# Optimization experiments

Hardware: AMD Instinct MI355X
Metric: run time of the kernel (lower is better)

Reference implementation:

```python
import jax, jax.numpy as jnp
import numpy as np

N_NODES = 100000
N_EDGES = 3200000
IN_CH, HIDDEN, OUT_CH = 256, 16, 16


def setup_inputs() -> dict:
    key = jax.random.key(0)
    k1, k2, k3, k4, k5, k6 = jax.random.split(key, 6)
    x = jax.random.normal(k1, (N_NODES, IN_CH), dtype=jnp.float32)
    edge_index = jax.random.randint(k2, (2, N_EDGES), 0, N_NODES, dtype=jnp.int64)
    W1 = jax.random.normal(k3, (IN_CH, HIDDEN), dtype=jnp.float32) * (1.0 / np.sqrt(IN_CH))
    b1 = jax.random.normal(k4, (HIDDEN,), dtype=jnp.float32) * 0.01
    W2 = jax.random.normal(k5, (HIDDEN, OUT_CH), dtype=jnp.float32) * (1.0 / np.sqrt(HIDDEN))
    b2 = jax.random.normal(k6, (OUT_CH,), dtype=jnp.float32) * 0.01
    return {"x": x, "edge_index": edge_index, "W1": W1, "b1": b1, "W2": W2, "b2": b2}


def gcn_layer(x, edge_index, W, b):
    # Linear projection: [N, in] @ [in, out] + b
    h = x @ W + b
    source, target = edge_index[0], edge_index[1]
    n = x.shape[0]
    # degree of target nodes (in-degree), symmetric normalization (Kipf & Welling 2017)
    deg = jax.ops.segment_sum(jnp.ones_like(target, dtype=h.dtype), target, num_segments=n)
    deg_inv_sqrt = jnp.where(deg > 0, jax.lax.rsqrt(jnp.maximum(deg, 1.0)), 0.0)
    norm = deg_inv_sqrt[source] * deg_inv_sqrt[target]  # [E]
    # gather-scale-scatter: msg = norm * h[source], aggregated by add at target
    msgs = norm[:, None] * h[source]  # [E, out]
    return jax.ops.segment_sum(msgs, target, num_segments=n)


def reference(x, edge_index, W1, b1, W2, b2):
    h = jax.nn.sigmoid(gcn_layer(x, edge_index, W1, b1))
    return jax.nn.sigmoid(gcn_layer(h, edge_index, W2, b2))
```

## Files before the change

kernel.cpp:

```cpp
#include <hip/hip_runtime.h>
#include <hip/hip_bf16.h>

#define IN_CH 256
#define HID 16
#define BS 256
#define CAP 9216
#define CHUNK 4096
#define PBLK 512
#define EPT (CHUNK/PBLK)
#define SORT_CAP CAP

typedef __attribute__((ext_vector_type(8))) short bf16x8;
typedef __attribute__((ext_vector_type(4))) float floatx4;

static __device__ __forceinline__ short f2bf(float f) {
    __hip_bfloat16 h = __float2bfloat16(f);
    return *reinterpret_cast<short*>(&h);
}

static __device__ __forceinline__ void acc8(float* a, uint4 v) {
    unsigned w;
    w = v.x;
    a[0] += __uint_as_float(w << 16);
    a[1] += __uint_as_float(w & 0xffff0000u);
    w = v.y;
    a[2] += __uint_as_float(w << 16);
    a[3] += __uint_as_float(w & 0xffff0000u);
    w = v.z;
    a[4] += __uint_as_float(w << 16);
    a[5] += __uint_as_float(w & 0xffff0000u);
    w = v.w;
    a[6] += __uint_as_float(w << 16);
    a[7] += __uint_as_float(w & 0xffff0000u);
}

__global__ __launch_bounds__(PBLK) void k_part(
        const int* __restrict__ src, const int* __restrict__ tgt,
        int* __restrict__ gcursor, unsigned int* __restrict__ csr, int E, int nbuk) {
    __shared__ int lcount[512];
    __shared__ int lexcl[512];
    __shared__ int gspan[512];
    __shared__ unsigned int sepk[CHUNK];
    __shared__ unsigned short sbuk[CHUNK];
    __shared__ int stot;
    int t = threadIdx.x;
    int base = blockIdx.x * CHUNK;

    lcount[t] = 0;
    __syncthreads();

    int ebuk[EPT], eofs[EPT];
    unsigned epk[EPT];
#pragma unroll
    for (int k = 0; k < EPT; k++) {
        int e = base + t + k * PBLK;
        if (e < E) {
            int s  = __builtin_nontemporal_load(src + e);
            int tg = __builtin_nontemporal_load(tgt + e);
            ebuk[k] = tg >> 8;
            epk[k] = ((unsigned)s << 8) | (unsigned)(tg & 255);
            eofs[k] = atomicAdd(&lcount[ebuk[k]], 1);
        } else {
            ebuk[k] = -1;
        }
    }
    __syncthreads();
    int v = lcount[t];
    lexcl[t] = v;
    __syncthreads();
    for (int off = 1; off < 512; off <<= 1) {
        int a = (t >= off) ? lexcl[t - off] : 0;
        __syncthreads();
        lexcl[t] += a;
        __syncthreads();
    }
    int inc = lexcl[t];
    if (t == 511) stot = inc;
    if (t < nbuk && v > 0) gspan[t] = atomicAdd(&gcursor[t], v);
    __syncthreads();
    lexcl[t] = inc - v;
    __syncthreads();
#pragma unroll
    for (int k = 0; k < EPT; k++) {
        if (ebuk[k] >= 0) {
            int sp = lexcl[ebuk[k]] + eofs[k];
            sepk[sp] = epk[k];
            sbuk[sp] = (unsigned short)ebuk[k];
        }
    }
    __syncthreads();
    int total = stot;
    for (int p = t; p < total; p += PBLK) {
        int buk = sbuk[p];
        int gp = gspan[buk] + (p - lexcl[buk]);
        if (gp < CAP)
            csr[(size_t)buk * CAP + gp] = sepk[p];
    }
}

__global__ __launch_bounds__(512, 4) void k_sortgemm(
        const unsigned int* __restrict__ csr, const int* __restrict__ gcursor,
        const float* __restrict__ x, const float* __restrict__ W1,
        const float* __restrict__ b1,
        int* __restrict__ csr2, int* __restrict__ rowptr,
        int* __restrict__ deg, float* __restrict__ dis,
        short* __restrict__ h1, int N) {
    __shared__ int lcnt[256];
    __shared__ int lscan[256];
    __shared__ float sdis[256];
    __shared__ int ssrc[SORT_CAP];
    int t = threadIdx.x, b = blockIdx.x;
    int start = b * CAP;
    int cnt = min(gcursor[b], CAP);
    int end = start + cnt;

    if (t < 256) lcnt[t] = 0;
    __syncthreads();
    for (int p = start + t; p < end; p += 512) atomicAdd(&lcnt[csr[p] & 255], 1);
    __syncthreads();
    int d = 0;
    if (t < 256) { d = lcnt[t]; lscan[t] = d; }
    __syncthreads();
    for (int off = 1; off < 256; off <<= 1) {
        int a = 0;
        if (t < 256 && t >= off) a = lscan[t - off];
        __syncthreads();
        if (t < 256) lscan[t] += a;
        __syncthreads();
    }
    if (t < 256) {
        int excl = lscan[t] - d;
        int n = b * BS + t;
        float dv = (d > 0) ? rsqrtf((float)d) : 0.0f;
        sdis[t] = dv;
        if (n < N) {
            rowptr[n] = start + excl;
            deg[n] = d;
            dis[n] = dv;
        }
        lcnt[t] = excl;
    }
    __syncthreads();
    for (int p = start + t; p < end; p += 512) {
        unsigned pk = csr[p];
        int pos = atomicAdd(&lcnt[pk & 255], 1);
        ssrc[pos] = (int)(pk >> 8);
    }
    __syncthreads();
    for (int i = t; i < cnt; i += 512) csr2[start + i] = ssrc[i];

    {
        int lane = t & 63, wave = t >> 6;
        int mc = lane & 15, q = lane >> 4;
        bf16x8 bfrag[8];
#pragma unroll
        for (int kb = 0; kb < 8; kb++) {
#pragma unroll
            for (int j = 0; j < 8; j++)
                bfrag[kb][j] = f2bf(W1[(kb * 32 + q * 8 + j) * HID + mc]);
        }
        float bias = b1[mc];
#pragma unroll
        for (int r2 = 0; r2 < 2; r2++) {
            int nb = b * BS + (wave * 2 + r2) * 16;
            if (nb < N) {
                const float* xrow = x + (size_t)(nb + mc) * IN_CH;
                floatx4 acc = {0.f, 0.f, 0.f, 0.f};
#pragma unroll
                for (int kb = 0; kb < 8; kb++) {
                    const floatx4* p = (const floatx4*)(xrow + kb * 32 + q * 8);
                    floatx4 v0 = __builtin_nontemporal_load(p);
                    floatx4 v1 = __builtin_nontemporal_load(p + 1);
                    bf16x8 afrag;
#pragma unroll
                    for (int j = 0; j < 4; j++) {
                        afrag[j]     = f2bf(v0[j]);
                        afrag[j + 4] = f2bf(v1[j]);
                    }
                    acc = __builtin_amdgcn_mfma_f32_16x16x32_bf16(afrag, bfrag[kb], acc, 0, 0, 0);
                }
#pragma unroll
                for (int r = 0; r < 4; r++) {
                    int node = nb + q * 4 + r;
                    h1[(size_t)node * HID + mc] = f2bf((acc[r] + bias) * sdis[node - b * BS]);
                }
            }
        }
    }
}

__global__ __launch_bounds__(256) void k_agg_mid(
        const short* __restrict__ h1, const int* __restrict__ csr2,
        const int* __restrict__ rowptr, const int* __restrict__ deg,
        const float* __restrict__ dis,
        const float* __restrict__ W2, const float* __restrict__ b2,
        short* __restrict__ h2, int N) {
    __shared__ float w2s[256];
    __shared__ float b2s[16];
    __shared__ float sv[32][17];
    int t = threadIdx.x;
    w2s[t] = W2[t];
    if (t < 16) b2s[t] = b2[t];
    int nl  = t >> 3;
    int sub = t & 7;
    int cg  = sub & 1;
    int par = sub >> 1;
    int n = blockIdx.x * 32 + nl;

    float a[8] = {0.f, 0.f, 0.f, 0.f, 0.f, 0.f, 0.f, 0.f};
    float d = 0.f;
    if (n < N) {
        d = dis[n];
        int start = rowptr[n], cnt = deg[n];
        const short* hb = h1 + 8 * cg;
        int i = start + par, end = start + cnt;
        for (; i + 4 < end; i += 8) {
            int s0 = csr2[i], s1 = csr2[i + 4];
            uint4 v0 = *(const uint4*)(hb + 16 * (size_t)s0);
            uint4 v1 = *(const uint4*)(hb + 16 * (size_t)s1);
            acc8(a, v0); acc8(a, v1);
        }
        if (i < end) {
            uint4 v = *(const uint4*)(hb + 16 * (size_t)csr2[i]);
            acc8(a, v);
        }
    }
#pragma unroll
    for (int j = 0; j < 8; j++) {
        a[j] += __shfl_xor(a[j], 2);
        a[j] += __shfl_xor(a[j], 4);
    }
    sv[nl][8 * cg + 2 * par]     = 1.0f / (1.0f + __expf(-d * a[2 * par]));
    sv[nl][8 * cg + 2 * par + 1] = 1.0f / (1.0f + __expf(-d * a[2 * par + 1]));
    __syncthreads();
    if (n < N) {
        int oc = sub * 2;
        float o0 = b2s[oc], o1 = b2s[oc + 1];
#pragma unroll
        for (int k = 0; k < 16; k++) {
            float s = sv[nl][k];
            o0 += s * w2s[k * 16 + oc];
            o1 += s * w2s[k * 16 + oc + 1];
        }
        unsigned pk = ((unsigned)(unsigned short)f2bf(o1 * d) << 16)
                    | (unsigned)(unsigned short)f2bf(o0 * d);
        *(unsigned int*)(h2 + 16 * (size_t)n + oc) = pk;
    }
}

__global__ __launch_bounds__(256) void k_agg_out(
        const short* __restrict__ h2, const int* __restrict__ csr2,
        const int* __restrict__ rowptr, const int* __restrict__ deg,
        const float* __restrict__ dis, float* __restrict__ out, int N) {
    int t = threadIdx.x;
    int nl  = t >> 3;
    int sub = t & 7;
    int cg  = sub & 1;
    int par = sub >> 1;
    int n = blockIdx.x * 32 + nl;
    if (n >= N) return;
    float d = dis[n];
    int start = rowptr[n], cnt = deg[n];
    float a[8] = {0.f, 0.f, 0.f, 0.f, 0.f, 0.f, 0.f, 0.f};
    const short* hb = h2 + 8 * cg;
    int i = start + par, end = start + cnt;
    for (; i + 4 < end; i += 8) {
        int s0 = csr2[i], s1 = csr2[i + 4];
        uint4 v0 = *(const uint4*)(hb + 16 * (size_t)s0);
        uint4 v1 = *(const uint4*)(hb + 16 * (size_t)s1);
        acc8(a, v0); acc8(a, v1);
    }
    if (i < end) {
        uint4 v = *(const uint4*)(hb + 16 * (size_t)csr2[i]);
        acc8(a, v);
    }
#pragma unroll
    for (int j = 0; j < 8; j++) {
        a[j] += __shfl_xor(a[j], 2);
        a[j] += __shfl_xor(a[j], 4);
    }
    float2 o;
    o.x = 1.0f / (1.0f + __expf(-d * a[2 * par]));
    o.y = 1.0f / (1.0f + __expf(-d * a[2 * par + 1]));
    *(float2*)(out + 16 * (size_t)n + 8 * cg + 2 * par) = o;
}

extern "C" void kernel_launch(void* const* d_in, const int* in_sizes, int n_in,
                              void* d_out, int out_size, void* d_ws, size_t ws_size,
                              hipStream_t stream) {
    const float* x  = (const float*)d_in[0];
    const int*   ei = (const int*)d_in[1];
    const float* W1 = (const float*)d_in[2];
    const float* b1 = (const float*)d_in[3];
    const float* W2 = (const float*)d_in[4];
    const float* b2 = (const float*)d_in[5];
    float* out = (float*)d_out;

    int N = in_sizes[0] / IN_CH;
    int E = in_sizes[1] / 2;
    const int* src = ei;
    const int* tgt = ei + E;

    int NBUK = (N + BS - 1) / BS;

    char* ws = (char*)d_ws;
    auto align256 = [](size_t v) { return (v + 255) & ~(size_t)255; };
    size_t off = 0;
    int*          gcursor = (int*)(ws + off);          off += align256(512 * sizeof(int));
    unsigned int* csr     = (unsigned int*)(ws + off); off += align256((size_t)NBUK * CAP * sizeof(unsigned int));
    int*          csr2    = (int*)(ws + off);          off += align256((size_t)NBUK * CAP * sizeof(int));
    int*          rowptr  = (int*)(ws + off);          off += align256((size_t)N * sizeof(int));
    int*          deg     = (int*)(ws + off);          off += align256((size_t)N * sizeof(int));
    float*        dis     = (float*)(ws + off);        off += align256((size_t)N * sizeof(float));
    short*        h1      = (short*)(ws + off);        off += align256((size_t)N * HID * sizeof(short));
    short*        h2      = (short*)(ws + off);        off += align256((size_t)N * HID * sizeof(short));

    int grid_part = (E + CHUNK - 1) / CHUNK;
    int grid_ag   = (N + 31) / 32;

    hipMemsetAsync(gcursor, 0, 512 * sizeof(int), stream);
    k_part    <<<grid_part, PBLK, 0, stream>>>(src, tgt, gcursor, csr, E, NBUK);
    k_sortgemm<<<NBUK, 512, 0, stream>>>(csr, gcursor, x, W1, b1,
                                         csr2, rowptr, deg, dis, h1, N);
    k_agg_mid <<<grid_ag, 256, 0, stream>>>(h1, csr2, rowptr, deg, dis, W2, b2, h2, N);
    k_agg_out <<<grid_ag, 256, 0, stream>>>(h2, csr2, rowptr, deg, dis, out, N);
}
```

Baseline: 265.6 us.

## Store layer-1 features as FP8 and enlarge partition chunk size

The layer-1 projected features h1 are now stored as FP8 (one byte per channel) instead of bf16. That halves the gather traffic in the first aggregation, and each thread decodes a full 16-channel row with packed fp8-to-f32 conversions. The reduction across the 8 lanes per node becomes a butterfly transpose-reduce so each lane ends up owning two channels. The partition chunk size per block is also doubled. FP8 storage of the normalized features adds substantial quantization error, which may break accuracy tolerances.

Result: faster. 255.7 us (-3.7%).

```diff
diff --git a/kernel.cpp b/kernel.cpp
--- a/kernel.cpp
+++ b/kernel.cpp
@@ -5,13 +5,14 @@
 #define HID 16
 #define BS 256
 #define CAP 9216
-#define CHUNK 4096
+#define CHUNK 8192
 #define PBLK 512
 #define EPT (CHUNK/PBLK)
 #define SORT_CAP CAP
 
 typedef __attribute__((ext_vector_type(8))) short bf16x8;
 typedef __attribute__((ext_vector_type(4))) float floatx4;
+typedef __attribute__((ext_vector_type(2))) float floatx2;
 
 static __device__ __forceinline__ short f2bf(float f) {
     __hip_bfloat16 h = __float2bfloat16(f);
@@ -34,6 +35,18 @@
     a[7] += __uint_as_float(w & 0xffff0000u);
 }
 
+static __device__ __forceinline__ void dec16(float* a, uint4 v) {
+    floatx2 f;
+    f = __builtin_amdgcn_cvt_pk_f32_fp8((int)v.x, false); a[0] += f[0];  a[1] += f[1];
+    f = __builtin_amdgcn_cvt_pk_f32_fp8((int)v.x, true ); a[2] += f[0];  a[3] += f[1];
+    f = __builtin_amdgcn_cvt_pk_f32_fp8((int)v.y, false); a[4] += f[0];  a[5] += f[1];
+    f = __builtin_amdgcn_cvt_pk_f32_fp8((int)v.y, true ); a[6] += f[0];  a[7] += f[1];
+    f = __builtin_amdgcn_cvt_pk_f32_fp8((int)v.z, false); a[8] += f[0];  a[9] += f[1];
+    f = __builtin_amdgcn_cvt_pk_f32_fp8((int)v.z, true ); a[10] += f[0]; a[11] += f[1];
+    f = __builtin_amdgcn_cvt_pk_f32_fp8((int)v.w, false); a[12] += f[0]; a[13] += f[1];
+    f = __builtin_amdgcn_cvt_pk_f32_fp8((int)v.w, true ); a[14] += f[0]; a[15] += f[1];
+}
+
 __global__ __launch_bounds__(PBLK) void k_part(
         const int* __restrict__ src, const int* __restrict__ tgt,
         int* __restrict__ gcursor, unsigned int* __restrict__ csr, int E, int nbuk) {
@@ -104,7 +117,7 @@
         const float* __restrict__ b1,
         int* __restrict__ csr2, int* __restrict__ rowptr,
         int* __restrict__ deg, float* __restrict__ dis,
-        short* __restrict__ h1, int N) {
+        unsigned char* __restrict__ h1, int N) {
     __shared__ int lcnt[256];
     __shared__ int lscan[256];
     __shared__ float sdis[256];
@@ -182,7 +195,9 @@
 #pragma unroll
                 for (int r = 0; r < 4; r++) {
                     int node = nb + q * 4 + r;
-                    h1[(size_t)node * HID + mc] = f2bf((acc[r] + bias) * sdis[node - b * BS]);
+                    float val = (acc[r] + bias) * sdis[node - b * BS];
+                    int pkv = __builtin_amdgcn_cvt_pk_fp8_f32(val, val, 0, false);
+                    h1[(size_t)node * HID + mc] = (unsigned char)(pkv & 0xff);
                 }
             }
         }
@@ -190,7 +205,7 @@
 }
 
 __global__ __launch_bounds__(256) void k_agg_mid(
-        const short* __restrict__ h1, const int* __restrict__ csr2,
+        const unsigned char* __restrict__ h1, const int* __restrict__ csr2,
         const int* __restrict__ rowptr, const int* __restrict__ deg,
         const float* __restrict__ dis,
         const float* __restrict__ W2, const float* __restrict__ b2,
@@ -203,35 +218,50 @@
     if (t < 16) b2s[t] = b2[t];
     int nl  = t >> 3;
     int sub = t & 7;
-    int cg  = sub & 1;
-    int par = sub >> 1;
     int n = blockIdx.x * 32 + nl;
 
-    float a[8] = {0.f, 0.f, 0.f, 0.f, 0.f, 0.f, 0.f, 0.f};
+    float a[16] = {0.f, 0.f, 0.f, 0.f, 0.f, 0.f, 0.f, 0.f,
+                   0.f, 0.f, 0.f, 0.f, 0.f, 0.f, 0.f, 0.f};
     float d = 0.f;
     if (n < N) {
         d = dis[n];
         int start = rowptr[n], cnt = deg[n];
-        const short* hb = h1 + 8 * cg;
-        int i = start + par, end = start + cnt;
-        for (; i + 4 < end; i += 8) {
-            int s0 = csr2[i], s1 = csr2[i + 4];
-            uint4 v0 = *(const uint4*)(hb + 16 * (size_t)s0);
-            uint4 v1 = *(const uint4*)(hb + 16 * (size_t)s1);
-            acc8(a, v0); acc8(a, v1);
+        int i = start + sub, end = start + cnt;
+        for (; i + 8 < end; i += 16) {
+            int s0 = csr2[i], s1 = csr2[i + 8];
+            uint4 v0 = *(const uint4*)(h1 + 16 * (size_t)s0);
+            uint4 v1 = *(const uint4*)(h1 + 16 * (size_t)s1);
+            dec16(a, v0); dec16(a, v1);
         }
         if (i < end) {
-            uint4 v = *(const uint4*)(hb + 16 * (size_t)csr2[i]);
-            acc8(a, v);
-        }
-    }
+            uint4 v = *(const uint4*)(h1 + 16 * (size_t)csr2[i]);
+            dec16(a, v);
+        }
+    }
+    float r8[8];
 #pragma unroll
     for (int j = 0; j < 8; j++) {
-        a[j] += __shfl_xor(a[j], 2);
-        a[j] += __shfl_xor(a[j], 4);
-    }
-    sv[nl][8 * cg + 2 * par]     = 1.0f / (1.0f + __expf(-d * a[2 * par]));
-    sv[nl][8 * cg + 2 * par + 1] = 1.0f / (1.0f + __expf(-d * a[2 * par + 1]));
+        float kept = (sub & 1) ? a[j + 8] : a[j];
+        float sent = (sub & 1) ? a[j] : a[j + 8];
+        r8[j] = kept + __shfl_xor(sent, 1);
+    }
+    float r4[4];
+#pragma unroll
+    for (int j = 0; j < 4; j++) {
+        float kept = (sub & 2) ? r8[j + 4] : r8[j];
+        float sent = (sub & 2) ? r8[j] : r8[j + 4];
+        r4[j] = kept + __shfl_xor(sent, 2);
+    }
+    float r2v[2];
+#pragma unroll
+    for (int j = 0; j < 2; j++) {
+        float kept = (sub & 4) ? r4[j + 2] : r4[j];
+        float sent = (sub & 4) ? r4[j] : r4[j + 2];
+        r2v[j] = kept + __shfl_xor(sent, 4);
+    }
+    int cbase = 8 * (sub & 1) + 4 * ((sub >> 1) & 1) + 2 * ((sub >> 2) & 1);
+    sv[nl][cbase]     = 1.0f / (1.0f + __expf(-d * r2v[0]));
+    sv[nl][cbase + 1] = 1.0f / (1.0f + __expf(-d * r2v[1]));
     __syncthreads();
     if (n < N) {
         int oc = sub * 2;
@@ -306,14 +336,14 @@
     char* ws = (char*)d_ws;
     auto align256 = [](size_t v) { return (v + 255) & ~(size_t)255; };
     size_t off = 0;
-    int*          gcursor = (int*)(ws + off);          off += align256(512 * sizeof(int));
-    unsigned int* csr     = (unsigned int*)(ws + off); off += align256((size_t)NBUK * CAP * sizeof(unsigned int));
-    int*          csr2    = (int*)(ws + off);          off += align256((size_t)NBUK * CAP * sizeof(int));
-    int*          rowptr  = (int*)(ws + off);          off += align256((size_t)N * sizeof(int));
-    int*          deg     = (int*)(ws + off);          off += align256((size_t)N * sizeof(int));
-    float*        dis     = (float*)(ws + off);        off += align256((size_t)N * sizeof(float));
-    short*        h1      = (short*)(ws + off);        off += align256((size_t)N * HID * sizeof(short));
-    short*        h2      = (short*)(ws + off);        off += align256((size_t)N * HID * sizeof(short));
+    int*           gcursor = (int*)(ws + off);           off += align256(512 * sizeof(int));
+    unsigned int*  csr     = (unsigned int*)(ws + off);  off += align256((size_t)NBUK * CAP * sizeof(unsigned int));
+    int*           csr2    = (int*)(ws + off);           off += align256((size_t)NBUK * CAP * sizeof(int));
+    int*           rowptr  = (int*)(ws + off);           off += align256((size_t)N * sizeof(int));
+    int*           deg     = (int*)(ws + off);           off += align256((size_t)N * sizeof(int));
+    float*         dis     = (float*)(ws + off);         off += align256((size_t)N * sizeof(float));
+    unsigned char* h1      = (unsigned char*)(ws + off); off += align256((size_t)N * HID * sizeof(unsigned char));
+    short*         h2      = (short*)(ws + off);         off += align256((size_t)N * HID * sizeof(short));
 
     int grid_part = (E + CHUNK - 1) / CHUNK;
     int grid_ag   = (N + 31) / 32;
```
